# Performance work log

Hardware: AMD Instinct MI355X
Metric: run time of the kernel (lower is better)

## Reference

```python
import jax, jax.numpy as jnp
import numpy as np

MARGIN = 0.3
N = 16384


def setup_inputs() -> dict:
    key = jax.random.key(0)
    k1, k2 = jax.random.split(key)
    inputs = jax.random.normal(k1, (N,), dtype=jnp.float32)
    targets = jax.random.randint(k2, (N,), 0, 2, dtype=jnp.int64)
    return {"inputs": inputs, "targets": targets}


def reference(inputs, targets):
    # Original: a = inputs[targets==1], b = inputs[targets==0];
    # all pairs (i, j): MarginRankingLoss(sigmoid(a_i), sigmoid(b_j), y=1)
    #   = mean_ij relu(margin - (sigmoid(a_i) - sigmoid(b_j)))
    # Expressed as a masked N x N broadcast so shapes stay static (jit-safe).
    s = jax.nn.sigmoid(inputs)  # [N]
    pos = (targets == 1)        # anchors-positive side
    neg = (targets == 0)        # negative side
    # hinge[i, j] = relu(margin - (s_i - s_j)) for pos i, neg j
    hinge = jax.nn.relu(MARGIN - (s[:, None] - s[None, :]))  # [N, N]
    mask = pos[:, None] & neg[None, :]                        # [N, N]
    num_pairs = jnp.sum(pos) * jnp.sum(neg)
    total = jnp.sum(jnp.where(mask, hinge, 0.0))
    return total / num_pairs.astype(s.dtype)
```

## Files before the change

kernel.cpp:

```cpp
#include <hip/hip_runtime.h>
#include <hip/hip_bf16.h>
#include <math.h>

#define MARGIN 0.3f
#define PAIR_BLOCKS 512


__global__ __launch_bounds__(256) void prep_compact_kernel(
        const float* __restrict__ inputs,
        const int* __restrict__ targets,
        float* __restrict__ a,
        float* __restrict__ b,
        unsigned int* __restrict__ pos_count,
        unsigned int* __restrict__ neg_count,
        int n) {
    __shared__ unsigned int wPos[4], wNeg[4];
    __shared__ unsigned int basePos, baseNeg;
    const int tid = threadIdx.x;
    const int i = blockIdx.x * 256 + tid;
    const bool valid = (i < n);
    float x = valid ? inputs[i] : 0.0f;
    int t = valid ? targets[i] : -1;
    float s = 1.0f / (1.0f + expf(-x));
    bool isPos = valid && (t == 1);
    bool isNeg = valid && (t == 0);

    unsigned long long mP = __ballot(isPos);
    unsigned long long mN = __ballot(isNeg);
    int lane = tid & 63, wave = tid >> 6;
    unsigned long long below = (1ull << lane) - 1ull;
    unsigned int pPre = (unsigned int)__popcll(mP & below);
    unsigned int nPre = (unsigned int)__popcll(mN & below);
    if (lane == 0) { wPos[wave] = (unsigned int)__popcll(mP);
                     wNeg[wave] = (unsigned int)__popcll(mN); }
    __syncthreads();
    if (tid == 0) {
        unsigned int tp = wPos[0] + wPos[1] + wPos[2] + wPos[3];
        unsigned int tn = wNeg[0] + wNeg[1] + wNeg[2] + wNeg[3];
        basePos = atomicAdd(pos_count, tp);
        baseNeg = atomicAdd(neg_count, tn);
    }
    __syncthreads();
    unsigned int wOffP = 0, wOffN = 0;
    for (int w = 0; w < wave; w++) { wOffP += wPos[w]; wOffN += wNeg[w]; }
    if (isPos) a[basePos + wOffP + pPre] = s;
    if (isNeg) b[baseNeg + wOffN + nPre] = MARGIN + s;
}

__global__ __launch_bounds__(256) void pair_reduce_kernel(
        const float* __restrict__ a,
        const float* __restrict__ b,
        const unsigned int* __restrict__ pos_count,
        const unsigned int* __restrict__ neg_count,
        double* __restrict__ total,
        unsigned int* __restrict__ done,
        float* __restrict__ out) {
    const int tid = threadIdx.x;
    const unsigned int P = *pos_count;
    const unsigned int Q = *neg_count;
    const unsigned int tilesI = (P + 511u) / 512u;
    const unsigned int tilesJ = (Q + 255u) / 256u;
    const unsigned int numTiles = tilesI * tilesJ;

    __shared__ float4 bs4[64];
    __shared__ double wsum[4];
    float* bs = (float*)bs4;

    double dlocal = 0.0;

    for (unsigned int tile = blockIdx.x; tile < numTiles; tile += gridDim.x) {
        unsigned int ti = tile / tilesJ;
        unsigned int tj = tile - ti * tilesJ;

        unsigned int j = tj * 256u + tid;
        bs[tid] = (j < Q) ? b[j] : -1e30f;

        unsigned int i0 = ti * 512u + tid;
        float a0 = (i0        < P) ? a[i0]       : 1e30f;
        float a1 = (i0 + 256u < P) ? a[i0 + 256] : 1e30f;
        __syncthreads();

        float c0 = 0.0f, c1 = 0.0f;
        #pragma unroll 8
        for (int q4 = 0; q4 < 64; q4++) {
            float4 b4 = bs4[q4];
            c0 += fmaxf(b4.x - a0, 0.0f);
            c0 += fmaxf(b4.y - a0, 0.0f);
            c0 += fmaxf(b4.z - a0, 0.0f);
            c0 += fmaxf(b4.w - a0, 0.0f);
            c1 += fmaxf(b4.x - a1, 0.0f);
            c1 += fmaxf(b4.y - a1, 0.0f);
            c1 += fmaxf(b4.z - a1, 0.0f);
            c1 += fmaxf(b4.w - a1, 0.0f);
        }
        dlocal += (double)c0 + (double)c1;
        __syncthreads();
    }

    for (int off = 32; off > 0; off >>= 1)
        dlocal += __shfl_down(dlocal, off, 64);

    int lane = tid & 63, wave = tid >> 6;
    if (lane == 0) wsum[wave] = dlocal;
    __syncthreads();
    if (tid == 0) {
        double bsum = wsum[0] + wsum[1] + wsum[2] + wsum[3];
        atomicAdd(total, bsum);
        __threadfence();
        unsigned int prev = atomicAdd(done, 1u);
        if (prev == gridDim.x - 1) {
            __threadfence();
            double T = atomicAdd(total, 0.0);
            double PQ = (double)P * (double)Q;
            out[0] = (PQ > 0.0) ? (float)(T / PQ) : 0.0f;
        }
    }
}

extern "C" void kernel_launch(void* const* d_in, const int* in_sizes, int n_in,
                              void* d_out, int out_size, void* d_ws, size_t ws_size,
                              hipStream_t stream) {
    const float* inputs  = (const float*)d_in[0];
    const int*   targets = (const int*)d_in[1];
    float* out = (float*)d_out;
    int n = in_sizes[0];

    char* ws = (char*)d_ws;
    double*       total     = (double*)(ws + 0);
    unsigned int* pos_count = (unsigned int*)(ws + 8);
    unsigned int* neg_count = (unsigned int*)(ws + 12);
    unsigned int* done      = (unsigned int*)(ws + 16);
    float*        a         = (float*)(ws + 32);
    float*        b         = (float*)(ws + 32 + (size_t)n * sizeof(float));

    hipMemsetAsync(d_ws, 0, 32, stream);

    int blocks = (n + 255) / 256;
    prep_compact_kernel<<<blocks, 256, 0, stream>>>(
        inputs, targets, a, b, pos_count, neg_count, n);

    pair_reduce_kernel<<<PAIR_BLOCKS, 256, 0, stream>>>(
        a, b, pos_count, neg_count, total, done, out);
}
```

Before: 76.86 us.

## Replace all-pairs hinge sum with single-block bucket sort and prefix sums

Replaces the O(P*Q) pairwise hinge reduction with an O(N) scheme. A single 1024-thread block computes sigmoids, bucket-sorts the smaller class into 1024 value bins in shared memory, and builds count and sum prefix arrays over them. Each element of the other class then gets its hinge contribution in closed form plus a scan of its own bin. This removes the memset, the second kernel launch and the quadratic work. In exchange everything runs on one CU, capacity is fixed at KMAX=8192 and EPT*NT=16384 elements, and the bin scan cost depends on how the values are distributed.

```diff
diff --git a/kernel.cpp b/kernel.cpp
--- a/kernel.cpp
+++ b/kernel.cpp
@@ -1,144 +1,177 @@
 #include <hip/hip_runtime.h>
-#include <hip/hip_bf16.h>
 #include <math.h>
 
 #define MARGIN 0.3f
-#define PAIR_BLOCKS 512
+#define NT   1024
+#define EPT  16
+#define NB   1024
+#define KMAX 8192
 
+__global__ __launch_bounds__(NT) void fused_loss_kernel(
+        const float* __restrict__ inputs,
+        const int*   __restrict__ targets,
+        float*       __restrict__ out,
+        int n)
+{
+    __shared__ float        sorted[KMAX];
+    __shared__ unsigned int binoff[NB];
+    __shared__ unsigned int start[NB + 1];
+    __shared__ double       psum[NB + 1];
+    __shared__ double       dscr[16];
+    __shared__ unsigned int uscr[16];
+    __shared__ unsigned int sPQ[2];
 
-__global__ __launch_bounds__(256) void prep_compact_kernel(
-        const float* __restrict__ inputs,
-        const int* __restrict__ targets,
-        float* __restrict__ a,
-        float* __restrict__ b,
-        unsigned int* __restrict__ pos_count,
-        unsigned int* __restrict__ neg_count,
-        int n) {
-    __shared__ unsigned int wPos[4], wNeg[4];
-    __shared__ unsigned int basePos, baseNeg;
-    const int tid = threadIdx.x;
-    const int i = blockIdx.x * 256 + tid;
-    const bool valid = (i < n);
-    float x = valid ? inputs[i] : 0.0f;
-    int t = valid ? targets[i] : -1;
-    float s = 1.0f / (1.0f + expf(-x));
-    bool isPos = valid && (t == 1);
-    bool isNeg = valid && (t == 0);
+    const int tid  = threadIdx.x;
+    const int lane = tid & 63;
+    const int wv   = tid >> 6;
 
-    unsigned long long mP = __ballot(isPos);
-    unsigned long long mN = __ballot(isNeg);
-    int lane = tid & 63, wave = tid >> 6;
-    unsigned long long below = (1ull << lane) - 1ull;
-    unsigned int pPre = (unsigned int)__popcll(mP & below);
-    unsigned int nPre = (unsigned int)__popcll(mN & below);
-    if (lane == 0) { wPos[wave] = (unsigned int)__popcll(mP);
-                     wNeg[wave] = (unsigned int)__popcll(mN); }
+    binoff[tid] = 0u;
+
+    float sv[EPT];
+    unsigned int posbits = 0u, negbits = 0u;
+    #pragma unroll
+    for (int k = 0; k < EPT; ++k) {
+        int idx = tid + k * NT;
+        float x = 0.0f; int t = -1;
+        if (idx < n) { x = inputs[idx]; t = targets[idx]; }
+        sv[k] = 1.0f / (1.0f + expf(-x));
+        if (t == 1) posbits |= (1u << k);
+        else if (t == 0) negbits |= (1u << k);
+    }
+
+    unsigned int cnt2 = ((unsigned int)__popc(posbits) << 16) | (unsigned int)__popc(negbits);
+    for (int off = 32; off > 0; off >>= 1)
+        cnt2 += __shfl_down(cnt2, off, 64);
+    if (lane == 0) uscr[wv] = cnt2;
     __syncthreads();
     if (tid == 0) {
-        unsigned int tp = wPos[0] + wPos[1] + wPos[2] + wPos[3];
-        unsigned int tn = wNeg[0] + wNeg[1] + wNeg[2] + wNeg[3];
-        basePos = atomicAdd(pos_count, tp);
-        baseNeg = atomicAdd(neg_count, tn);
+        unsigned int tot = 0u;
+        for (int w = 0; w < 16; ++w) tot += uscr[w];
+        sPQ[0] = tot >> 16; sPQ[1] = tot & 0xffffu;
     }
     __syncthreads();
-    unsigned int wOffP = 0, wOffN = 0;
-    for (int w = 0; w < wave; w++) { wOffP += wPos[w]; wOffN += wNeg[w]; }
-    if (isPos) a[basePos + wOffP + pPre] = s;
-    if (isNeg) b[baseNeg + wOffN + nPre] = MARGIN + s;
-}
+    const unsigned int P = sPQ[0], Q = sPQ[1];
+    if (P == 0u || Q == 0u) { if (tid == 0) out[0] = 0.0f; return; }
 
-__global__ __launch_bounds__(256) void pair_reduce_kernel(
-        const float* __restrict__ a,
-        const float* __restrict__ b,
-        const unsigned int* __restrict__ pos_count,
-        const unsigned int* __restrict__ neg_count,
-        double* __restrict__ total,
-        unsigned int* __restrict__ done,
-        float* __restrict__ out) {
-    const int tid = threadIdx.x;
-    const unsigned int P = *pos_count;
-    const unsigned int Q = *neg_count;
-    const unsigned int tilesI = (P + 511u) / 512u;
-    const unsigned int tilesJ = (Q + 255u) / 256u;
-    const unsigned int numTiles = tilesI * tilesJ;
+    const bool sortPos = (P <= Q);
+    const unsigned int K        = sortPos ? P : Q;
+    const unsigned int sortbits = sortPos ? posbits : negbits;
+    const unsigned int strmbits = sortPos ? negbits : posbits;
+    const float sortAdd = sortPos ? 0.0f : MARGIN;
+    const float strmAdd = sortPos ? MARGIN : 0.0f;
+    const float lo      = sortAdd;
+    const float scale   = (float)NB;
 
-    __shared__ float4 bs4[64];
-    __shared__ double wsum[4];
-    float* bs = (float*)bs4;
+    #pragma unroll
+    for (int k = 0; k < EPT; ++k) {
+        if (sortbits & (1u << k)) {
+            float v = sv[k] + sortAdd;
+            int b = (int)((v - lo) * scale);
+            b = min(max(b, 0), NB - 1);
+            atomicAdd(&binoff[b], 1u);
+        }
+    }
+    __syncthreads();
 
-    double dlocal = 0.0;
+    unsigned int c  = binoff[tid];
+    unsigned int iv = c;
+    for (int off = 1; off < 64; off <<= 1) {
+        unsigned int t = __shfl_up(iv, off, 64);
+        if (lane >= off) iv += t;
+    }
+    if (lane == 63) uscr[wv] = iv;
+    __syncthreads();
+    if (tid == 0) {
+        unsigned int accu = 0u;
+        for (int w = 0; w < 16; ++w) { unsigned int t = uscr[w]; uscr[w] = accu; accu += t; }
+    }
+    __syncthreads();
+    const unsigned int excl = uscr[wv] + iv - c;
+    start[tid] = excl;
+    if (tid == NT - 1) start[NB] = excl + c;
+    __syncthreads();
+    binoff[tid] = excl;
+    __syncthreads();
 
-    for (unsigned int tile = blockIdx.x; tile < numTiles; tile += gridDim.x) {
-        unsigned int ti = tile / tilesJ;
-        unsigned int tj = tile - ti * tilesJ;
+    #pragma unroll
+    for (int k = 0; k < EPT; ++k) {
+        if (sortbits & (1u << k)) {
+            float v = sv[k] + sortAdd;
+            int b = (int)((v - lo) * scale);
+            b = min(max(b, 0), NB - 1);
+            unsigned int p = atomicAdd(&binoff[b], 1u);
+            sorted[p] = v;
+        }
+    }
+    __syncthreads();
 
-        unsigned int j = tj * 256u + tid;
-        bs[tid] = (j < Q) ? b[j] : -1e30f;
+    double bsum = 0.0;
+    {
+        unsigned int s0 = start[tid], s1 = start[tid + 1];
+        for (unsigned int j = s0; j < s1; ++j) bsum += (double)sorted[j];
+    }
+    double dv = bsum;
+    for (int off = 1; off < 64; off <<= 1) {
+        double t = __shfl_up(dv, off, 64);
+        if (lane >= off) dv += t;
+    }
+    if (lane == 63) dscr[wv] = dv;
+    __syncthreads();
+    if (tid == 0) {
+        double accd = 0.0;
+        for (int w = 0; w < 16; ++w) { double t = dscr[w]; dscr[w] = accd; accd += t; }
+    }
+    __syncthreads();
+    const double dexcl = dscr[wv] + dv - bsum;
+    psum[tid] = dexcl;
+    if (tid == NT - 1) psum[NB] = dexcl + bsum;
+    __syncthreads();
 
-        unsigned int i0 = ti * 512u + tid;
-        float a0 = (i0        < P) ? a[i0]       : 1e30f;
-        float a1 = (i0 + 256u < P) ? a[i0 + 256] : 1e30f;
-        __syncthreads();
-
-        float c0 = 0.0f, c1 = 0.0f;
-        #pragma unroll 8
-        for (int q4 = 0; q4 < 64; q4++) {
-            float4 b4 = bs4[q4];
-            c0 += fmaxf(b4.x - a0, 0.0f);
-            c0 += fmaxf(b4.y - a0, 0.0f);
-            c0 += fmaxf(b4.z - a0, 0.0f);
-            c0 += fmaxf(b4.w - a0, 0.0f);
-            c1 += fmaxf(b4.x - a1, 0.0f);
-            c1 += fmaxf(b4.y - a1, 0.0f);
-            c1 += fmaxf(b4.z - a1, 0.0f);
-            c1 += fmaxf(b4.w - a1, 0.0f);
+    const double Stot = psum[NB];
+    double acc = 0.0;
+    #pragma unroll
+    for (int k = 0; k < EPT; ++k) {
+        if (strmbits & (1u << k)) {
+            float u = sv[k] + strmAdd;
+            int b = (int)((u - lo) * scale);
+            b = min(max(b, 0), NB - 1);
+            unsigned int s0 = start[b], s1 = start[b + 1];
+            if (sortPos) {
+                unsigned int cb = s0; double S = psum[b];
+                for (unsigned int j = s0; j < s1; ++j) {
+                    float vv = sorted[j];
+                    if (vv < u) { cb++; S += (double)vv; }
+                }
+                acc += (double)cb * (double)u - S;
+            } else {
+                unsigned int ch = K - s1; double S = Stot - psum[b + 1];
+                for (unsigned int j = s0; j < s1; ++j) {
+                    float vv = sorted[j];
+                    if (vv > u) { ch++; S += (double)vv; }
+                }
+                acc += S - (double)ch * (double)u;
+            }
         }
-        dlocal += (double)c0 + (double)c1;
-        __syncthreads();
     }
 
     for (int off = 32; off > 0; off >>= 1)
-        dlocal += __shfl_down(dlocal, off, 64);
-
-    int lane = tid & 63, wave = tid >> 6;
-    if (lane == 0) wsum[wave] = dlocal;
+        acc += __shfl_down(acc, off, 64);
+    __syncthreads();
+    if (lane == 0) dscr[wv] = acc;
     __syncthreads();
     if (tid == 0) {
-        double bsum = wsum[0] + wsum[1] + wsum[2] + wsum[3];
-        atomicAdd(total, bsum);
-        __threadfence();
-        unsigned int prev = atomicAdd(done, 1u);
-        if (prev == gridDim.x - 1) {
-            __threadfence();
-            double T = atomicAdd(total, 0.0);
-            double PQ = (double)P * (double)Q;
-            out[0] = (PQ > 0.0) ? (float)(T / PQ) : 0.0f;
-        }
+        double tot = 0.0;
+        for (int w = 0; w < 16; ++w) tot += dscr[w];
+        out[0] = (float)(tot / ((double)P * (double)Q));
     }
 }
 
 extern "C" void kernel_launch(void* const* d_in, const int* in_sizes, int n_in,
                               void* d_out, int out_size, void* d_ws, size_t ws_size,
                               hipStream_t stream) {
+    (void)n_in; (void)out_size; (void)d_ws; (void)ws_size;
     const float* inputs  = (const float*)d_in[0];
     const int*   targets = (const int*)d_in[1];
-    float* out = (float*)d_out;
     int n = in_sizes[0];
-
-    char* ws = (char*)d_ws;
-    double*       total     = (double*)(ws + 0);
-    unsigned int* pos_count = (unsigned int*)(ws + 8);
-    unsigned int* neg_count = (unsigned int*)(ws + 12);
-    unsigned int* done      = (unsigned int*)(ws + 16);
-    float*        a         = (float*)(ws + 32);
-    float*        b         = (float*)(ws + 32 + (size_t)n * sizeof(float));
-
-    hipMemsetAsync(d_ws, 0, 32, stream);
-
-    int blocks = (n + 255) / 256;
-    prep_compact_kernel<<<blocks, 256, 0, stream>>>(
-        inputs, targets, a, b, pos_count, neg_count, n);
-
-    pair_reduce_kernel<<<PAIR_BLOCKS, 256, 0, stream>>>(
-        a, b, pos_count, neg_count, total, done, out);
+    fused_loss_kernel<<<1, NT, 0, stream>>>(inputs, targets, (float*)d_out, n);
 }
```

Measured after the change: 94.13 us. 1.22x slower.
